# Kernel optimization log

Hardware: AMD Instinct MI355X
Metric: run time of the kernel (lower is better)

Reference implementation:

```python
import math
import jax, jax.numpy as jnp
import numpy as np

B, T, D = 512, 512, 256
ALPHA = 0.5
BETA = 0.9


def setup_inputs() -> dict:
    key = jax.random.key(0)
    ks = jax.random.split(key, 9)
    s = 1.0 / math.sqrt(D)
    return {
        "window_features": jax.random.normal(ks[0], (B, T, D), jnp.float32),
        "timestamps": jax.random.uniform(ks[1], (B, T), jnp.float32) * 86400.0 * 7,
        "prev_L": jax.random.normal(ks[2], (B, D), jnp.float32),
        "prev_M": jax.random.uniform(ks[3], (B, 1), jnp.float32),
        "pad_mask": jnp.zeros((B, T), jnp.bool_),
        "W_Q": jax.random.normal(ks[4], (D, D), jnp.float32) * s,
        "W_K": jax.random.normal(ks[5], (D, D), jnp.float32) * s,
        "W_V": jax.random.normal(ks[6], (D, D), jnp.float32) * s,
        "cls_w": jax.random.normal(ks[7], (1, 2 * D + 1), jnp.float32) * s,
        "cls_b": jnp.zeros((1,), jnp.float32),
    }


def reference(window_features, timestamps, prev_L, prev_M, pad_mask,
              W_Q, W_K, W_V, cls_w, cls_b):
    Bv, Tv, d = window_features.shape
    valid = ~pad_mask
    valid_f = valid.astype(window_features.dtype)              # [B,T]
    valid_count = jnp.clip(valid_f.sum(1, keepdims=True), 1.0)  # [B,1]

    # decay weights from recency (days)
    t_masked = jnp.where(pad_mask, -1e18, timestamps)
    t_max = t_masked.max(1, keepdims=True)                      # [B,1]
    dt = jnp.clip(t_max - timestamps, 0.0) / 86400.0
    lam = jnp.exp(-ALPHA * dt) * valid_f                        # [B,T]

    # mean-pooled query
    q = (window_features * valid_f[..., None]).sum(1) / valid_count  # [B,d]
    Q = q @ W_Q.T                                               # [B,d]
    K = jnp.einsum('btd,ed->bte', window_features, W_K)         # [B,T,d]
    V = jnp.einsum('btd,ed->bte', window_features, W_V)         # [B,T,d]

    scores = jnp.einsum('bd,btd->bt', Q, K) / math.sqrt(d)      # [B,T]
    scores = jnp.where(pad_mask, -1e9, scores)
    attn = jax.nn.softmax(scores, axis=-1)

    # decay-modulated reweighting + renormalization
    w = lam * attn
    w = w / (w.sum(1, keepdims=True) + 1e-8)

    L_t = jnp.einsum('bt,btd->bd', w, V)                        # [B,d]
    delta_t = L_t - prev_L
    M_t = BETA * prev_M + (1.0 - BETA) * jnp.linalg.norm(delta_t, axis=1, keepdims=True)
    T_event = jnp.concatenate([L_t, delta_t, M_t], axis=-1)     # [B,2d+1]
    p = (T_event @ cls_w.T + cls_b).squeeze(-1)                 # [B]
    return (p, T_event, L_t, M_t)
```

## Files before the change

### kernel.cpp

```cpp
#include <hip/hip_runtime.h>
#include <math.h>

#define ALPHA 0.5f
#define BETA 0.9f
#define Bsz 512
#define Tsz 512
#define Dsz 256
#define NCHUNK 4
#define CROWS (Tsz / NCHUNK)

__device__ __forceinline__ float wave_reduce_sum(float v) {
    v += __shfl_xor(v, 32, 64);
    v += __shfl_xor(v, 16, 64);
    v += __shfl_xor(v, 8, 64);
    v += __shfl_xor(v, 4, 64);
    v += __shfl_xor(v, 2, 64);
    v += __shfl_xor(v, 1, 64);
    return v;
}

__device__ __forceinline__ float wave_reduce_max(float v) {
    v = fmaxf(v, __shfl_xor(v, 32, 64));
    v = fmaxf(v, __shfl_xor(v, 16, 64));
    v = fmaxf(v, __shfl_xor(v, 8, 64));
    v = fmaxf(v, __shfl_xor(v, 4, 64));
    v = fmaxf(v, __shfl_xor(v, 2, 64));
    v = fmaxf(v, __shfl_xor(v, 1, 64));
    return v;
}

__global__ __launch_bounds__(256) void kA1(const float* __restrict__ x,
                                           const float* __restrict__ ts,
                                           const unsigned char* __restrict__ pad,
                                           float* __restrict__ qpart,
                                           float* __restrict__ cntp,
                                           float* __restrict__ tmaxp) {
    const int idx = blockIdx.x;
    const int b = idx >> 2, chunk = idx & 3;
    const int tid = threadIdx.x;
    const int w = tid >> 6, lane = tid & 63;
    const int t0 = chunk * CROWS;

    __shared__ float validS[CROWS];
    __shared__ float part[4][Dsz];
    __shared__ float red[8];

    float lmax = -3e38f, lcnt = 0.f;
    if (tid < CROWS) {
        bool v = (pad[(size_t)b * Tsz + t0 + tid] == 0);
        float tv = ts[(size_t)b * Tsz + t0 + tid];
        validS[tid] = v ? 1.f : 0.f;
        if (v) { lmax = tv; lcnt = 1.f; }
    }
    lmax = wave_reduce_max(lmax);
    lcnt = wave_reduce_sum(lcnt);
    if (lane == 0) { red[w] = lmax; red[4 + w] = lcnt; }
    __syncthreads();

    const float* xb = x + (size_t)b * Tsz * Dsz;
    float4 a0 = make_float4(0.f, 0.f, 0.f, 0.f);
    float4 a1 = a0, a2 = a0, a3 = a0;
    const int lb = w * 32;
    for (int i = 0; i < 32; i += 4) {
        const int lt = lb + i;
        const size_t g = (size_t)(t0 + lt) * Dsz + lane * 4;
        float4 x0 = *(const float4*)(xb + g);
        float4 x1 = *(const float4*)(xb + g + Dsz);
        float4 x2 = *(const float4*)(xb + g + 2 * Dsz);
        float4 x3 = *(const float4*)(xb + g + 3 * Dsz);
        const float v0 = validS[lt], v1 = validS[lt + 1], v2 = validS[lt + 2], v3 = validS[lt + 3];
        a0.x += v0 * x0.x; a0.y += v0 * x0.y; a0.z += v0 * x0.z; a0.w += v0 * x0.w;
        a1.x += v1 * x1.x; a1.y += v1 * x1.y; a1.z += v1 * x1.z; a1.w += v1 * x1.w;
        a2.x += v2 * x2.x; a2.y += v2 * x2.y; a2.z += v2 * x2.z; a2.w += v2 * x2.w;
        a3.x += v3 * x3.x; a3.y += v3 * x3.y; a3.z += v3 * x3.z; a3.w += v3 * x3.w;
    }
    part[w][lane * 4 + 0] = (a0.x + a1.x) + (a2.x + a3.x);
    part[w][lane * 4 + 1] = (a0.y + a1.y) + (a2.y + a3.y);
    part[w][lane * 4 + 2] = (a0.z + a1.z) + (a2.z + a3.z);
    part[w][lane * 4 + 3] = (a0.w + a1.w) + (a2.w + a3.w);
    __syncthreads();
    qpart[(size_t)idx * Dsz + tid] = (part[0][tid] + part[1][tid]) + (part[2][tid] + part[3][tid]);
    if (tid == 0) {
        tmaxp[idx] = fmaxf(fmaxf(red[0], red[1]), fmaxf(red[2], red[3]));
        cntp[idx] = (red[4] + red[5]) + (red[6] + red[7]);
    }
}

__global__ __launch_bounds__(256) void kA2(const float* __restrict__ qpart,
                                           const float* __restrict__ cntp,
                                           const float* __restrict__ tmaxp,
                                           const float* __restrict__ WQ,
                                           const float* __restrict__ WK,
                                           float* __restrict__ qk,
                                           float* __restrict__ tmax_out) {
    const int b = blockIdx.x;
    const int tid = threadIdx.x;
    __shared__ float qS[Dsz];
    __shared__ float QS[Dsz];
    __shared__ float cntS;

    if (tid == 0) {
        float tm = fmaxf(fmaxf(tmaxp[b * 4], tmaxp[b * 4 + 1]),
                         fmaxf(tmaxp[b * 4 + 2], tmaxp[b * 4 + 3]));
        cntS = fmaxf(cntp[b * 4] + cntp[b * 4 + 1] + cntp[b * 4 + 2] + cntp[b * 4 + 3], 1.f);
        tmax_out[b] = tm;
    }
    __syncthreads();
    qS[tid] = ((qpart[(size_t)(b * 4 + 0) * Dsz + tid] + qpart[(size_t)(b * 4 + 1) * Dsz + tid]) +
               (qpart[(size_t)(b * 4 + 2) * Dsz + tid] + qpart[(size_t)(b * 4 + 3) * Dsz + tid])) / cntS;
    __syncthreads();

    float Qi = 0.f;
    const float* wqrow = WQ + (size_t)tid * Dsz;
    #pragma unroll 4
    for (int d4 = 0; d4 < Dsz; d4 += 4) {
        float4 wv = *(const float4*)(wqrow + d4);
        Qi += wv.x * qS[d4] + wv.y * qS[d4 + 1] + wv.z * qS[d4 + 2] + wv.w * qS[d4 + 3];
    }
    QS[tid] = Qi;
    __syncthreads();

    float v = 0.f;
    #pragma unroll 8
    for (int e = 0; e < Dsz; ++e) {
        v += QS[e] * WK[(size_t)e * Dsz + tid];
    }
    qk[(size_t)b * Dsz + tid] = v * 0.0625f;
}

__global__ __launch_bounds__(256) void kB1(const float* __restrict__ x,
                                           const float* __restrict__ ts,
                                           const unsigned char* __restrict__ pad,
                                           const float* __restrict__ qk,
                                           const float* __restrict__ tmax_in,
                                           float* __restrict__ accp,
                                           float* __restrict__ Ep,
                                           float* __restrict__ Gp) {
    const int idx = blockIdx.x;
    const int b = idx >> 2, chunk = idx & 3;
    const int tid = threadIdx.x;
    const int w = tid >> 6, lane = tid & 63;
    const int t0 = chunk * CROWS;

    __shared__ float lamS[CROWS];
    __shared__ float okS[CROWS];
    __shared__ float accS[4][Dsz];
    __shared__ float EGS[8];

    const float tmax = tmax_in[b];
    if (tid < CROWS) {
        bool valid = (pad[(size_t)b * Tsz + t0 + tid] == 0);
        float dt = fmaxf(tmax - ts[(size_t)b * Tsz + t0 + tid], 0.f) * (1.f / 86400.f);
        lamS[tid] = valid ? __expf(-ALPHA * dt) : 0.f;
        okS[tid] = valid ? 1.f : 0.f;
    }
    __syncthreads();

    const float4 qk4 = *(const float4*)(qk + (size_t)b * Dsz + lane * 4);
    const float* xb = x + (size_t)b * Tsz * Dsz;
    float4 acc = make_float4(0.f, 0.f, 0.f, 0.f);
    float E = 0.f, G = 0.f;
    const int lb = w * 32;
    for (int i = 0; i < 32; i += 4) {
        const int lt = lb + i;
        const size_t g = (size_t)(t0 + lt) * Dsz + lane * 4;
        float4 x0 = *(const float4*)(xb + g);
        float4 x1 = *(const float4*)(xb + g + Dsz);
        float4 x2 = *(const float4*)(xb + g + 2 * Dsz);
        float4 x3 = *(const float4*)(xb + g + 3 * Dsz);
        float s0 = qk4.x * x0.x + qk4.y * x0.y + qk4.z * x0.z + qk4.w * x0.w;
        float s1 = qk4.x * x1.x + qk4.y * x1.y + qk4.z * x1.z + qk4.w * x1.w;
        float s2 = qk4.x * x2.x + qk4.y * x2.y + qk4.z * x2.z + qk4.w * x2.w;
        float s3 = qk4.x * x3.x + qk4.y * x3.y + qk4.z * x3.z + qk4.w * x3.w;
        #pragma unroll
        for (int off = 32; off >= 1; off >>= 1) {
            s0 += __shfl_xor(s0, off, 64);
            s1 += __shfl_xor(s1, off, 64);
            s2 += __shfl_xor(s2, off, 64);
            s3 += __shfl_xor(s3, off, 64);
        }
        float e0 = okS[lt + 0] * __expf(s0);
        float e1 = okS[lt + 1] * __expf(s1);
        float e2 = okS[lt + 2] * __expf(s2);
        float e3 = okS[lt + 3] * __expf(s3);
        float g0 = lamS[lt + 0] * e0;
        float g1 = lamS[lt + 1] * e1;
        float g2 = lamS[lt + 2] * e2;
        float g3 = lamS[lt + 3] * e3;
        E += (e0 + e1) + (e2 + e3);
        G += (g0 + g1) + (g2 + g3);
        acc.x += g0 * x0.x + g1 * x1.x + g2 * x2.x + g3 * x3.x;
        acc.y += g0 * x0.y + g1 * x1.y + g2 * x2.y + g3 * x3.y;
        acc.z += g0 * x0.z + g1 * x1.z + g2 * x2.z + g3 * x3.z;
        acc.w += g0 * x0.w + g1 * x1.w + g2 * x2.w + g3 * x3.w;
    }
    accS[w][lane * 4 + 0] = acc.x;
    accS[w][lane * 4 + 1] = acc.y;
    accS[w][lane * 4 + 2] = acc.z;
    accS[w][lane * 4 + 3] = acc.w;
    if (lane == 0) { EGS[w] = E; EGS[4 + w] = G; }
    __syncthreads();
    accp[(size_t)idx * Dsz + tid] = (accS[0][tid] + accS[1][tid]) + (accS[2][tid] + accS[3][tid]);
    if (tid == 0) {
        Ep[idx] = (EGS[0] + EGS[1]) + (EGS[2] + EGS[3]);
        Gp[idx] = (EGS[4] + EGS[5]) + (EGS[6] + EGS[7]);
    }
}

__global__ __launch_bounds__(256) void kB2(const float* __restrict__ accp,
                                           const float* __restrict__ Ep,
                                           const float* __restrict__ Gp,
                                           const float* __restrict__ WV,
                                           const float* __restrict__ prevL,
                                           const float* __restrict__ prevM,
                                           const float* __restrict__ clsw,
                                           const float* __restrict__ clsb,
                                           float* __restrict__ out) {
    const int b = blockIdx.x;
    const int tid = threadIdx.x;
    const int w = tid >> 6, lane = tid & 63;

    __shared__ float xwS[Dsz];
    __shared__ float red[4];
    __shared__ float red2[4];

    float E = (Ep[b * 4] + Ep[b * 4 + 1]) + (Ep[b * 4 + 2] + Ep[b * 4 + 3]);
    float G = (Gp[b * 4] + Gp[b * 4 + 1]) + (Gp[b * 4 + 2] + Gp[b * 4 + 3]);
    float denom = G + 1e-8f * E;
    float accd = (accp[(size_t)(b * 4 + 0) * Dsz + tid] + accp[(size_t)(b * 4 + 1) * Dsz + tid]) +
                 (accp[(size_t)(b * 4 + 2) * Dsz + tid] + accp[(size_t)(b * 4 + 3) * Dsz + tid]);
    xwS[tid] = (denom > 0.f) ? accd / denom : 0.f;
    __syncthreads();

    float Le = 0.f;
    const float* wvrow = WV + (size_t)tid * Dsz;
    #pragma unroll 4
    for (int d4 = 0; d4 < Dsz; d4 += 4) {
        float4 wv = *(const float4*)(wvrow + d4);
        Le += wv.x * xwS[d4] + wv.y * xwS[d4 + 1] + wv.z * xwS[d4 + 2] + wv.w * xwS[d4 + 3];
    }
    float delta = Le - prevL[(size_t)b * Dsz + tid];

    float ssq = wave_reduce_sum(delta * delta);
    if (lane == 0) red[w] = ssq;
    __syncthreads();
    float nrm = sqrtf((red[0] + red[1]) + (red[2] + red[3]));
    float M = BETA * prevM[b] + (1.f - BETA) * nrm;

    float pp = Le * clsw[tid] + delta * clsw[Dsz + tid];
    float psum = wave_reduce_sum(pp);
    if (lane == 0) red2[w] = psum;
    __syncthreads();

    float* out_p = out;
    float* out_T = out + Bsz;
    float* out_L = out + Bsz + (size_t)Bsz * (2 * Dsz + 1);
    float* out_M = out + Bsz + (size_t)Bsz * (2 * Dsz + 1) + (size_t)Bsz * Dsz;

    out_T[(size_t)b * (2 * Dsz + 1) + tid] = Le;
    out_T[(size_t)b * (2 * Dsz + 1) + Dsz + tid] = delta;
    out_L[(size_t)b * Dsz + tid] = Le;
    if (tid == 0) {
        float p = (red2[0] + red2[1]) + (red2[2] + red2[3]) + M * clsw[2 * Dsz] + clsb[0];
        out_p[b] = p;
        out_T[(size_t)b * (2 * Dsz + 1) + 2 * Dsz] = M;
        out_M[b] = M;
    }
}

extern "C" void kernel_launch(void* const* d_in, const int* in_sizes, int n_in,
                              void* d_out, int out_size, void* d_ws, size_t ws_size,
                              hipStream_t stream) {
    const float* x     = (const float*)d_in[0];
    const float* ts    = (const float*)d_in[1];
    const float* prevL = (const float*)d_in[2];
    const float* prevM = (const float*)d_in[3];
    const unsigned char* pad = (const unsigned char*)d_in[4];
    const float* WQ    = (const float*)d_in[5];
    const float* WK    = (const float*)d_in[6];
    const float* WV    = (const float*)d_in[7];
    const float* clsw  = (const float*)d_in[8];
    const float* clsb  = (const float*)d_in[9];

    float* ws = (float*)d_ws;
    float* qk    = ws;
    float* tmax  = qk + (size_t)Bsz * Dsz;
    float* qpart = tmax + Bsz;
    float* cntp  = qpart + (size_t)Bsz * NCHUNK * Dsz;
    float* tmaxp = cntp + (size_t)Bsz * NCHUNK;
    float* accp  = tmaxp + (size_t)Bsz * NCHUNK;
    float* Ep    = accp + (size_t)Bsz * NCHUNK * Dsz;
    float* Gp    = Ep + (size_t)Bsz * NCHUNK;

    kA1<<<Bsz * NCHUNK, 256, 0, stream>>>(x, ts, pad, qpart, cntp, tmaxp);
    kA2<<<Bsz, 256, 0, stream>>>(qpart, cntp, tmaxp, WQ, WK, qk, tmax);
    kB1<<<Bsz * NCHUNK, 256, 0, stream>>>(x, ts, pad, qk, tmax, accp, Ep, Gp);
    kB2<<<Bsz, 256, 0, stream>>>(accp, Ep, Gp, WV, prevL, prevM, clsw, clsb, (float*)d_out);
}
```

Baseline: 458.8 us.

## Write bf16 copy of features in first pass and read it reversed in second

The first pass now also writes a bf16-packed copy of the window features to workspace. The attention-accumulation kernel reads this half-size copy instead of the fp32 input, processing 8 rows per iteration. It also walks blocks in reverse order to reuse recently written data from cache. This trades extra write traffic and reduced precision in the scores and weighted sum for smaller second-pass reads.

Result: no change. 467.9 us (+2.0%).

```diff
diff --git a/kernel.cpp b/kernel.cpp
--- a/kernel.cpp
+++ b/kernel.cpp
@@ -29,9 +29,18 @@
     return v;
 }
 
+__device__ __forceinline__ unsigned pack_bf16(float a, float b) {
+    unsigned ua = __float_as_uint(a);
+    unsigned ub = __float_as_uint(b);
+    ua += 0x7fffu + ((ua >> 16) & 1u);
+    ub += 0x7fffu + ((ub >> 16) & 1u);
+    return (ua >> 16) | (ub & 0xffff0000u);
+}
+
 __global__ __launch_bounds__(256) void kA1(const float* __restrict__ x,
                                            const float* __restrict__ ts,
                                            const unsigned char* __restrict__ pad,
+                                           unsigned* __restrict__ xb16,
                                            float* __restrict__ qpart,
                                            float* __restrict__ cntp,
                                            float* __restrict__ tmaxp) {
@@ -58,6 +67,7 @@
     __syncthreads();
 
     const float* xb = x + (size_t)b * Tsz * Dsz;
+    unsigned* ob = xb16 + (size_t)b * Tsz * (Dsz / 2);
     float4 a0 = make_float4(0.f, 0.f, 0.f, 0.f);
     float4 a1 = a0, a2 = a0, a3 = a0;
     const int lb = w * 32;
@@ -73,6 +83,11 @@
         a1.x += v1 * x1.x; a1.y += v1 * x1.y; a1.z += v1 * x1.z; a1.w += v1 * x1.w;
         a2.x += v2 * x2.x; a2.y += v2 * x2.y; a2.z += v2 * x2.z; a2.w += v2 * x2.w;
         a3.x += v3 * x3.x; a3.y += v3 * x3.y; a3.z += v3 * x3.z; a3.w += v3 * x3.w;
+        const size_t o = (size_t)(t0 + lt) * (Dsz / 2) + lane * 2;
+        *(uint2*)(ob + o)                = make_uint2(pack_bf16(x0.x, x0.y), pack_bf16(x0.z, x0.w));
+        *(uint2*)(ob + o + (Dsz / 2))    = make_uint2(pack_bf16(x1.x, x1.y), pack_bf16(x1.z, x1.w));
+        *(uint2*)(ob + o + 2 * (Dsz / 2)) = make_uint2(pack_bf16(x2.x, x2.y), pack_bf16(x2.z, x2.w));
+        *(uint2*)(ob + o + 3 * (Dsz / 2)) = make_uint2(pack_bf16(x3.x, x3.y), pack_bf16(x3.z, x3.w));
     }
     part[w][lane * 4 + 0] = (a0.x + a1.x) + (a2.x + a3.x);
     part[w][lane * 4 + 1] = (a0.y + a1.y) + (a2.y + a3.y);
@@ -128,7 +143,7 @@
     qk[(size_t)b * Dsz + tid] = v * 0.0625f;
 }
 
-__global__ __launch_bounds__(256) void kB1(const float* __restrict__ x,
+__global__ __launch_bounds__(256) void kB1(const unsigned* __restrict__ xb16,
                                            const float* __restrict__ ts,
                                            const unsigned char* __restrict__ pad,
                                            const float* __restrict__ qk,
@@ -136,7 +151,7 @@
                                            float* __restrict__ accp,
                                            float* __restrict__ Ep,
                                            float* __restrict__ Gp) {
-    const int idx = blockIdx.x;
+    const int idx = (int)gridDim.x - 1 - blockIdx.x;
     const int b = idx >> 2, chunk = idx & 3;
     const int tid = threadIdx.x;
     const int w = tid >> 6, lane = tid & 63;
@@ -157,42 +172,39 @@
     __syncthreads();
 
     const float4 qk4 = *(const float4*)(qk + (size_t)b * Dsz + lane * 4);
-    const float* xb = x + (size_t)b * Tsz * Dsz;
+    const unsigned* xb = xb16 + (size_t)b * Tsz * (Dsz / 2);
     float4 acc = make_float4(0.f, 0.f, 0.f, 0.f);
     float E = 0.f, G = 0.f;
     const int lb = w * 32;
-    for (int i = 0; i < 32; i += 4) {
+    for (int i = 0; i < 32; i += 8) {
         const int lt = lb + i;
-        const size_t g = (size_t)(t0 + lt) * Dsz + lane * 4;
-        float4 x0 = *(const float4*)(xb + g);
-        float4 x1 = *(const float4*)(xb + g + Dsz);
-        float4 x2 = *(const float4*)(xb + g + 2 * Dsz);
-        float4 x3 = *(const float4*)(xb + g + 3 * Dsz);
-        float s0 = qk4.x * x0.x + qk4.y * x0.y + qk4.z * x0.z + qk4.w * x0.w;
-        float s1 = qk4.x * x1.x + qk4.y * x1.y + qk4.z * x1.z + qk4.w * x1.w;
-        float s2 = qk4.x * x2.x + qk4.y * x2.y + qk4.z * x2.z + qk4.w * x2.w;
-        float s3 = qk4.x * x3.x + qk4.y * x3.y + qk4.z * x3.z + qk4.w * x3.w;
+        uint2 u[8];
+        #pragma unroll
+        for (int r = 0; r < 8; ++r)
+            u[r] = *(const uint2*)(xb + (size_t)(t0 + lt + r) * (Dsz / 2) + lane * 2);
+        float xf[8][4];
+        float s[8];
+        #pragma unroll
+        for (int r = 0; r < 8; ++r) {
+            xf[r][0] = __uint_as_float(u[r].x << 16);
+            xf[r][1] = __uint_as_float(u[r].x & 0xffff0000u);
+            xf[r][2] = __uint_as_float(u[r].y << 16);
+            xf[r][3] = __uint_as_float(u[r].y & 0xffff0000u);
+            s[r] = qk4.x * xf[r][0] + qk4.y * xf[r][1] + qk4.z * xf[r][2] + qk4.w * xf[r][3];
+        }
         #pragma unroll
         for (int off = 32; off >= 1; off >>= 1) {
-            s0 += __shfl_xor(s0, off, 64);
-            s1 += __shfl_xor(s1, off, 64);
-            s2 += __shfl_xor(s2, off, 64);
-            s3 += __shfl_xor(s3, off, 64);
+            #pragma unroll
+            for (int r = 0; r < 8; ++r) s[r] += __shfl_xor(s[r], off, 64);
         }
-        float e0 = okS[lt + 0] * __expf(s0);
-        float e1 = okS[lt + 1] * __expf(s1);
-        float e2 = okS[lt + 2] * __expf(s2);
-        float e3 = okS[lt + 3] * __expf(s3);
-        float g0 = lamS[lt + 0] * e0;
-        float g1 = lamS[lt + 1] * e1;
-        float g2 = lamS[lt + 2] * e2;
-        float g3 = lamS[lt + 3] * e3;
-        E += (e0 + e1) + (e2 + e3);
-        G += (g0 + g1) + (g2 + g3);
-        acc.x += g0 * x0.x + g1 * x1.x + g2 * x2.x + g3 * x3.x;
-        acc.y += g0 * x0.y + g1 * x1.y + g2 * x2.y + g3 * x3.y;
-        acc.z += g0 * x0.z + g1 * x1.z + g2 * x2.z + g3 * x3.z;
-        acc.w += g0 * x0.w + g1 * x1.w + g2 * x2.w + g3 * x3.w;
+        #pragma unroll
+        for (int r = 0; r < 8; ++r) {
+            float e = okS[lt + r] * __expf(s[r]);
+            float g = lamS[lt + r] * e;
+            E += e; G += g;
+            acc.x += g * xf[r][0]; acc.y += g * xf[r][1];
+            acc.z += g * xf[r][2]; acc.w += g * xf[r][3];
+        }
     }
     accS[w][lane * 4 + 0] = acc.x;
     accS[w][lane * 4 + 1] = acc.y;
@@ -282,8 +294,9 @@
     const float* clsw  = (const float*)d_in[8];
     const float* clsb  = (const float*)d_in[9];
 
-    float* ws = (float*)d_ws;
-    float* qk    = ws;
+    unsigned* xb16 = (unsigned*)d_ws;
+    float* wsf  = (float*)(xb16 + (size_t)Bsz * Tsz * (Dsz / 2));
+    float* qk    = wsf;
     float* tmax  = qk + (size_t)Bsz * Dsz;
     float* qpart = tmax + Bsz;
     float* cntp  = qpart + (size_t)Bsz * NCHUNK * Dsz;
@@ -292,8 +305,8 @@
     float* Ep    = accp + (size_t)Bsz * NCHUNK * Dsz;
     float* Gp    = Ep + (size_t)Bsz * NCHUNK;
 
-    kA1<<<Bsz * NCHUNK, 256, 0, stream>>>(x, ts, pad, qpart, cntp, tmaxp);
+    kA1<<<Bsz * NCHUNK, 256, 0, stream>>>(x, ts, pad, xb16, qpart, cntp, tmaxp);
     kA2<<<Bsz, 256, 0, stream>>>(qpart, cntp, tmaxp, WQ, WK, qk, tmax);
-    kB1<<<Bsz * NCHUNK, 256, 0, stream>>>(x, ts, pad, qk, tmax, accp, Ep, Gp);
+    kB1<<<Bsz * NCHUNK, 256, 0, stream>>>(xb16, ts, pad, qk, tmax, accp, Ep, Gp);
     kB2<<<Bsz, 256, 0, stream>>>(accp, Ep, Gp, WV, prevL, prevM, clsw, clsb, (float*)d_out);
 }
```
